# Performance work log

Measured on AMD Instinct MI355X. Metric: run time of the kernel, lower is better.

## Reference

```python
import jax, jax.numpy as jnp
import numpy as np

V = 100277      # VOCAB_SIZE
SCR = 64        # SCRATCH_SLOTS
STEPS = 8       # MAX_STEPS_LIMIT
H = 8           # num_heads (hard-coded in UniversalReasoner)
NEG = -1e9


def _layernorm(x, s, b, eps=1e-6):
    mu = x.mean(-1, keepdims=True)
    var = ((x - mu) ** 2).mean(-1, keepdims=True)
    return (x - mu) * jax.lax.rsqrt(var + eps) * s + b


def setup_inputs() -> dict:
    key = jax.random.key(0)
    ks = jax.random.split(key, 16)
    D = 1024
    n = lambda k, shape, sc=0.02: jax.random.normal(k, shape, dtype=jnp.float32) * sc
    return {
        "tokens": jax.random.randint(ks[0], (16, 128), 0, V),
        "embed": n(ks[1], (V, D)),
        "time_embed": n(ks[2], (STEPS + 1, D)),
        "scratch": n(ks[3], (1, SCR, D)),
        "wq": n(ks[4], (D, D)), "bq": jnp.zeros((D,), jnp.float32),
        "wk": n(ks[5], (D, D)), "bk": jnp.zeros((D,), jnp.float32),
        "wv": n(ks[6], (D, D)), "bv": jnp.zeros((D,), jnp.float32),
        "wo": n(ks[7], (D, D)), "bo": jnp.zeros((D,), jnp.float32),
        "ln1_s": jnp.ones((D,), jnp.float32), "ln1_b": jnp.zeros((D,), jnp.float32),
        "ln2_s": jnp.ones((D,), jnp.float32), "ln2_b": jnp.zeros((D,), jnp.float32),
        "w1": n(ks[8], (D, 4 * D)), "b1": jnp.zeros((4 * D,), jnp.float32),
        "w2": n(ks[9], (4 * D, D)), "b2": jnp.zeros((D,), jnp.float32),
        "halt_w": n(ks[10], (D, 1)), "halt_b": jnp.zeros((1,), jnp.float32),
        "dec_w": n(ks[11], (D, V)), "dec_b": jnp.zeros((V,), jnp.float32),
    }


def reference(tokens, embed, time_embed, scratch, wq, bq, wk, bk, wv, bv, wo, bo,
              ln1_s, ln1_b, ln2_s, ln2_b, w1, b1, w2, b2, halt_w, halt_b, dec_w, dec_b):
    B, S = tokens.shape
    D = embed.shape[1]
    hd = D // H
    T = S + SCR                     # seq + scratch slots
    scale = hd ** -0.5

    # RoPE caches (matches 10000**(arange(0,hd,2)/hd) in the module)
    inv_freq = 1.0 / 10000.0 ** (jnp.arange(0, hd, 2, dtype=jnp.float32) / hd)
    t = jnp.arange(T, dtype=jnp.float32)
    freqs = jnp.outer(t, inv_freq)              # [T, hd/2]
    sin = jnp.sin(freqs); cos = jnp.cos(freqs)
    sin_ext = jnp.stack([sin, sin], -1).reshape(T, hd)[None, :, None, :]
    cos_ext = jnp.stack([cos, cos], -1).reshape(T, hd)[None, :, None, :]

    # hybrid mask: causal for the seq part, fully-visible rows for scratch tokens
    causal = jnp.tril(jnp.ones((T, T), dtype=bool))
    mask = causal.at[S:, :].set(True)[None, None, :, :]   # [1,1,T,T]

    def rotate(x):  # x: [B,T,H,hd]
        xe, xo = x[..., 0::2], x[..., 1::2]
        xr = jnp.stack([-xo, xe], -1).reshape(x.shape)
        return x * cos_ext + xr * sin_ext

    def block(x):   # one StandardReasoningBlock on [B,T,D]
        h = _layernorm(x, ln1_s, ln1_b)
        q = (h @ wq + bq).reshape(B, T, H, hd)
        k = (h @ wk + bk).reshape(B, T, H, hd)
        v = (h @ wv + bv).reshape(B, T, H, hd)
        q, k = rotate(q), rotate(k)
        logits = jnp.einsum('bshd,bthd->bhst', q, k) * scale
        logits = jnp.where(mask, logits, NEG)
        w = jax.nn.softmax(logits, axis=-1)
        o = jnp.einsum('bhst,bthd->bshd', w, v).reshape(B, T, D)
        x = x + (o @ wo + bo)
        h2 = _layernorm(x, ln2_s, ln2_b)
        x = x + jax.nn.gelu(h2 @ w1 + b1, approximate=True) @ w2 + b2
        return x

    z0 = jnp.concatenate([embed[tokens], jnp.tile(scratch, (B, 1, 1))], axis=1)  # [B,T,D]

    def step(z, i):
        zt = z + time_embed[i][None, None, :]
        nz = block(zt)
        halt = jax.nn.sigmoid((nz[:, S:, :] @ halt_w + halt_b).mean(axis=(1, 2)))  # [B]
        return nz, halt

    final_z, halts = jax.lax.scan(step, z0, jnp.arange(STEPS))   # halts: [STEPS, B]
    logits_out = final_z[:, :S, :] @ dec_w + dec_b               # [B,S,V]
    return logits_out, halts
```

## Files before the change

kernel.cpp:

```cpp
#include <hip/hip_runtime.h>
#include <hip/hip_bf16.h>
#include <math.h>


typedef float  f32x4  __attribute__((ext_vector_type(4)));
typedef __bf16 bf16x8 __attribute__((ext_vector_type(8)));
typedef __bf16 bf16x4 __attribute__((ext_vector_type(4)));

static constexpr int BB   = 16;
static constexpr int S    = 128;
static constexpr int SCR  = 64;
static constexpr int T    = 192;
static constexpr int D    = 1024;
static constexpr int H    = 8;
static constexpr int HD   = 128;
static constexpr int DFF  = 4096;
static constexpr int NSTEP= 8;
static constexpr int V    = 100277;
static constexpr int ROWS = BB * T;
static constexpr int MD   = BB * S;
static constexpr long long LOGITS = (long long)BB * S * V;

#define DEV __device__ __forceinline__

DEV void gload16(const __bf16* g, __bf16* l) {
  __builtin_amdgcn_global_load_lds(
      (__attribute__((address_space(1))) void*)(g),
      (__attribute__((address_space(3))) void*)(l), 16, 0, 0);
}

template <int EPI>
__global__ __launch_bounds__(256) void k_gemm(
    const __bf16* __restrict__ A, long long sA, int ldA, int M,
    const __bf16* __restrict__ Bt, long long sB, int ldB, int N, int K,
    const float* __restrict__ bias, void* __restrict__ C, long long sC,
    int ldC) {
  const int bz = blockIdx.z;
  const __bf16* Ab;
  const __bf16* Bb;
  if constexpr (EPI == 4) {
    Ab = A + (size_t)bz * K;
    Bb = Bt + (size_t)bz * K;
  } else {
    Ab = A + (size_t)bz * sA;
    Bb = Bt + (size_t)bz * sB;
  }
  const int tm = blockIdx.y * 128, tn = blockIdx.x * 128;
  const int tid = threadIdx.x;
  const int lane = tid & 63, wv = tid >> 6;
  const int wr = wv >> 1, wc = wv & 1;

  __shared__ __bf16 As[2][128 * 32];
  __shared__ __bf16 Bs[2][128 * 32];

  f32x4 acc[4][4];
#pragma unroll
  for (int m = 0; m < 4; m++)
#pragma unroll
    for (int n = 0; n < 4; n++) acc[m][n] = (f32x4)(0.f);

  const int lrow = lane >> 2;
  const int lcol = (((lane & 3) ^ (lrow & 3)) * 8);
  int arow[2], brow[2];
#pragma unroll
  for (int c2 = 0; c2 < 2; c2++) {
    const int ch = wv * 2 + c2;
    int ar = tm + ch * 16 + lrow; if (ar > M - 1) ar = M - 1;
    int br = tn + ch * 16 + lrow; if (br > N - 1) br = N - 1;
    arow[c2] = ar; brow[c2] = br;
  }

  auto stage = [&](int buf, int kk) {
#pragma unroll
    for (int c2 = 0; c2 < 2; c2++) {
      const int ch = wv * 2 + c2;
      gload16(Ab + (size_t)arow[c2] * ldA + kk + lcol, &As[buf][ch * 512]);
      gload16(Bb + (size_t)brow[c2] * ldB + kk + lcol, &Bs[buf][ch * 512]);
    }
  };

  const int rsl = (((lane >> 4) ^ (lane & 3)) * 8);
  auto compute = [&](int cur) {
    bf16x8 af[4], bfv[4];
#pragma unroll
    for (int m = 0; m < 4; m++)
      af[m] = *(const bf16x8*)&As[cur][(wr * 64 + m * 16 + (lane & 15)) * 32 + rsl];
#pragma unroll
    for (int n = 0; n < 4; n++)
      bfv[n] = *(const bf16x8*)&Bs[cur][(wc * 64 + n * 16 + (lane & 15)) * 32 + rsl];
    asm volatile("s_waitcnt lgkmcnt(0)" ::: "memory");
    __builtin_amdgcn_sched_barrier(0);
    __builtin_amdgcn_s_barrier();
#pragma unroll
    for (int m = 0; m < 4; m++)
#pragma unroll
      for (int n = 0; n < 4; n++)
        acc[m][n] = __builtin_amdgcn_mfma_f32_16x16x32_bf16(af[m], bfv[n],
                                                            acc[m][n], 0, 0, 0);
  };

  const int niter = K >> 5;
  stage(0, 0);
  for (int it = 0; it < niter - 1; ++it) {
    const int cur = it & 1;
    stage(cur ^ 1, (it + 1) << 5);
    asm volatile("s_waitcnt vmcnt(4)" ::: "memory");
    __builtin_amdgcn_s_barrier();
    compute(cur);
  }
  asm volatile("s_waitcnt vmcnt(0)" ::: "memory");
  __builtin_amdgcn_s_barrier();
  compute((niter - 1) & 1);

  const int r0 = tm + wr * 64, c0 = tn + wc * 64;
#pragma unroll
  for (int n = 0; n < 4; n++) {
    const int c = c0 + n * 16 + (lane & 15);
    if (c >= N) continue;
    const float bsv = (bias && (EPI != 4 || bz == 0)) ? bias[c] : 0.f;
#pragma unroll
    for (int m = 0; m < 4; m++) {
      const int rb = r0 + m * 16 + ((lane >> 4) << 2);
#pragma unroll
      for (int j = 0; j < 4; j++) {
        const int r = rb + j;
        if (r >= M) continue;
        float x = acc[m][n][j] + bsv;
        if constexpr (EPI == 3) {
          const int b = bz >> 3, hh = bz & 7;
          ((__bf16*)C)[((size_t)(b * T + r)) * D + hh * HD + c] = (__bf16)x;
        } else if constexpr (EPI == 4) {
          atomicAdd((float*)C + (size_t)r * ldC + c, x);
        } else {
          const size_t idx = (size_t)bz * sC + (size_t)r * ldC + c;
          if constexpr (EPI == 2) {
            const float u = x;
            const float gl =
                0.5f * u * (1.f + tanhf(0.7978845608f * (u + 0.044715f * u * u * u)));
            ((__bf16*)C)[idx] = (__bf16)gl;
          } else if constexpr (EPI == 1) {
            ((float*)C)[idx] += x;
          } else {
            ((float*)C)[idx] = x;
          }
        }
      }
    }
  }
}

static constexpr int DEC_NT = (V + 127) / 128;
static constexpr int DEC_NWG = 16 * DEC_NT;

__global__ __launch_bounds__(256) void k_dec(const __bf16* __restrict__ A,
                                             const __bf16* __restrict__ Bt,
                                             const float* __restrict__ bias,
                                             float* __restrict__ C) {
  const int bid = blockIdx.x;
  const int swz = (bid & 7) * (DEC_NWG / 8) + (bid >> 3);
  const int tm = (swz & 15) * 128, tn = (swz >> 4) * 128;
  const int tid = threadIdx.x;
  const int lane = tid & 63, wv = tid >> 6;
  const int wr = wv >> 1, wc = wv & 1;

  __shared__ __bf16 sAB[2][2][4096];
  float* cbuf = (float*)sAB;

  f32x4 acc[4][4];
#pragma unroll
  for (int m = 0; m < 4; m++)
#pragma unroll
    for (int n = 0; n < 4; n++) acc[m][n] = (f32x4)(0.f);

  const int lrow = lane >> 2;
  const int lcol = (((lane & 3) ^ (lrow & 3)) * 8);
  int arow[2], brow[2];
#pragma unroll
  for (int c2 = 0; c2 < 2; c2++) {
    const int ch = wv * 2 + c2;
    arow[c2] = tm + ch * 16 + lrow;
    int br = tn + ch * 16 + lrow; if (br > V - 1) br = V - 1;
    brow[c2] = br;
  }

  auto stage = [&](int buf, int kk) {
#pragma unroll
    for (int c2 = 0; c2 < 2; c2++) {
      const int ch = wv * 2 + c2;
      gload16(A + (size_t)arow[c2] * D + kk + lcol, &sAB[buf][0][ch * 512]);
      gload16(Bt + (size_t)brow[c2] * D + kk + lcol, &sAB[buf][1][ch * 512]);
    }
  };

  const int rsl = (((lane >> 4) ^ (lane & 3)) * 8);
  auto compute = [&](int cur) {
    bf16x8 af[4], bfv[4];
#pragma unroll
    for (int m = 0; m < 4; m++)
      af[m] = *(const bf16x8*)&sAB[cur][0][(wr * 64 + m * 16 + (lane & 15)) * 32 + rsl];
#pragma unroll
    for (int n = 0; n < 4; n++)
      bfv[n] = *(const bf16x8*)&sAB[cur][1][(wc * 64 + n * 16 + (lane & 15)) * 32 + rsl];
    asm volatile("s_waitcnt lgkmcnt(0)" ::: "memory");
    __builtin_amdgcn_sched_barrier(0);
    __builtin_amdgcn_s_barrier();
#pragma unroll
    for (int m = 0; m < 4; m++)
#pragma unroll
      for (int n = 0; n < 4; n++)
        acc[m][n] = __builtin_amdgcn_mfma_f32_16x16x32_bf16(af[m], bfv[n],
                                                            acc[m][n], 0, 0, 0);
  };

  stage(0, 0);
  for (int it = 0; it < D / 32 - 1; ++it) {
    const int cur = it & 1;
    stage(cur ^ 1, (it + 1) << 5);
    asm volatile("s_waitcnt vmcnt(4)" ::: "memory");
    __builtin_amdgcn_s_barrier();
    compute(cur);
  }
  asm volatile("s_waitcnt vmcnt(0)" ::: "memory");
  __builtin_amdgcn_s_barrier();
  compute((D / 32 - 1) & 1);
  __syncthreads();

  const int l15 = lane & 15, g4 = lane >> 4;
  const bool full = (tn + 128 <= V);
  for (int pass = 0; pass < 2; ++pass) {
    if (pass) __syncthreads();
    if (wr == pass) {
#pragma unroll
      for (int n = 0; n < 4; n++) {
        const int col = wc * 64 + n * 16 + l15;
        const float bsv = (tn + col < V) ? bias[tn + col] : 0.f;
#pragma unroll
        for (int m = 0; m < 4; m++) {
#pragma unroll
          for (int j = 0; j < 4; j++) {
            const int row = m * 16 + g4 * 4 + j;
            const int slot = (col >> 2) ^ (row & 7);
            cbuf[row * 128 + slot * 4 + (col & 3)] = acc[m][n][j] + bsv;
          }
        }
      }
    }
    __syncthreads();
    const int rbase = tm + pass * 64;
    if (full) {
      const int c8 = tid & 7;
#pragma unroll
      for (int rr = 0; rr < 2; ++rr) {
        const int row = rr * 32 + (tid >> 3);
#pragma unroll
        for (int i = 0; i < 4; ++i) {
          const int ps = (c8 ^ (row & 7)) + i * 8;
          const f32x4 v = *(const f32x4*)&cbuf[row * 128 + ps * 4];
          *(f32x4*)&C[(size_t)(rbase + row) * V + tn + (c8 + i * 8) * 4] = v;
        }
      }
    } else {
      for (int idx = tid; idx < 64 * 128; idx += 256) {
        const int row = idx >> 7, col = idx & 127;
        if (tn + col < V)
          C[(size_t)(rbase + row) * V + tn + col] =
              cbuf[row * 128 + (((col >> 2) ^ (row & 7)) << 2) + (col & 3)];
      }
    }
  }
}

__global__ __launch_bounds__(256) void k_transpose(const float* __restrict__ in,
                                                   __bf16* __restrict__ out,
                                                   int R, int C) {
  __shared__ __bf16 tile[32][33];
  const int c0 = blockIdx.x * 32, r0 = blockIdx.y * 32;
  const int tx = threadIdx.x & 31, ty = threadIdx.x >> 5;
#pragma unroll
  for (int i = 0; i < 32; i += 8) {
    const int r = r0 + ty + i, c = c0 + tx;
    tile[ty + i][tx] = (r < R && c < C) ? (__bf16)in[(size_t)r * C + c] : (__bf16)0.f;
  }
  __syncthreads();
  const int oc = threadIdx.x >> 3, rch = (threadIdx.x & 7) * 4;
  const int occ = c0 + oc, orr = r0 + rch;
  if (occ < C && orr + 3 < R) {
    bf16x4 v;
#pragma unroll
    for (int j = 0; j < 4; j++) v[j] = tile[rch + j][oc];
    *(bf16x4*)(out + (size_t)occ * R + orr) = v;
  }
}

__global__ __launch_bounds__(256) void k_concat_bias(const float* bq,
                                                     const float* bk,
                                                     const float* bv,
                                                     float* out) {
  const int i = blockIdx.x * 256 + threadIdx.x;
  if (i < D) { out[i] = bq[i]; out[D + i] = bk[i]; out[2 * D + i] = bv[i]; }
}

__global__ __launch_bounds__(256) void k_rope_table(float* __restrict__ ct,
                                                    float* __restrict__ st) {
  const int i = blockIdx.x * 256 + threadIdx.x;
  if (i < T * 64) {
    const int t = i >> 6, j = i & 63;
    const float inv = expf(-((float)(2 * j) * (1.f / 128.f)) * 9.210340371976184f);
    const float ang = (float)t * inv;
    ct[i] = cosf(ang);
    st[i] = sinf(ang);
  }
}

__global__ __launch_bounds__(256) void k_build_z(const int* __restrict__ tokens,
                                                 const float* __restrict__ embed,
                                                 const float* __restrict__ scratch,
                                                 float* __restrict__ z) {
  const int row = blockIdx.x;
  const int b = row / T, t = row % T;
  const float* src = (t < S) ? embed + (size_t)tokens[b * S + t] * D
                             : scratch + (size_t)(t - S) * D;
  ((float4*)(z + (size_t)row * D))[threadIdx.x] =
      ((const float4*)src)[threadIdx.x];
}

template <bool ADDT>
__global__ __launch_bounds__(256) void k_ln(float* __restrict__ z,
                                            const float* __restrict__ te,
                                            const float* __restrict__ gs,
                                            const float* __restrict__ gb,
                                            __bf16* __restrict__ h) {
  const int row = blockIdx.x, tid = threadIdx.x;
  float* zp = z + (size_t)row * D;
  float4 x = ((float4*)zp)[tid];
  if (ADDT) {
    const float4 t4 = ((const float4*)te)[tid];
    x.x += t4.x; x.y += t4.y; x.z += t4.z; x.w += t4.w;
    ((float4*)zp)[tid] = x;
  }
  float s = x.x + x.y + x.z + x.w;
  float s2 = x.x * x.x + x.y * x.y + x.z * x.z + x.w * x.w;
#pragma unroll
  for (int o = 32; o; o >>= 1) { s += __shfl_xor(s, o); s2 += __shfl_xor(s2, o); }
  __shared__ float rs[4], rq[4];
  const int wv = tid >> 6, ln = tid & 63;
  if (!ln) { rs[wv] = s; rq[wv] = s2; }
  __syncthreads();
  s = rs[0] + rs[1] + rs[2] + rs[3];
  s2 = rq[0] + rq[1] + rq[2] + rq[3];
  const float mu = s * (1.f / D);
  const float var = s2 * (1.f / D) - mu * mu;
  const float rinv = 1.0f / sqrtf(var + 1e-6f);
  const int c = tid * 4;
  const float4 g4 = ((const float4*)gs)[tid];
  const float4 b4 = ((const float4*)gb)[tid];
  bf16x4 o4;
  o4[0] = (__bf16)((x.x - mu) * rinv * g4.x + b4.x);
  o4[1] = (__bf16)((x.y - mu) * rinv * g4.y + b4.y);
  o4[2] = (__bf16)((x.z - mu) * rinv * g4.z + b4.z);
  o4[3] = (__bf16)((x.w - mu) * rinv * g4.w + b4.w);
  *(bf16x4*)(h + (size_t)row * D + c) = o4;
}

__global__ __launch_bounds__(256) void k_rope_pack(
    const float* __restrict__ qkv, const float* __restrict__ ct,
    const float* __restrict__ st, __bf16* __restrict__ q,
    __bf16* __restrict__ k, __bf16* __restrict__ vT) {
  const int row = blockIdx.x;
  const int b = row / T, t = row % T;
  const int i0 = threadIdx.x * 4;
  const int hh = i0 >> 7, d = i0 & 127, j0 = d >> 1;
  const float* base = qkv + (size_t)row * 3072;
  const float4 qv = *(const float4*)(base + i0);
  const float4 kv = *(const float4*)(base + D + i0);
  const float4 vv = *(const float4*)(base + 2 * D + i0);
  const float c0 = ct[t * 64 + j0], s0 = st[t * 64 + j0];
  const float c1 = ct[t * 64 + j0 + 1], s1 = st[t * 64 + j0 + 1];
  bf16x4 qo, ko;
  qo[0] = (__bf16)(qv.x * c0 - qv.y * s0);
  qo[1] = (__bf16)(qv.y * c0 + qv.x * s0);
  qo[2] = (__bf16)(qv.z * c1 - qv.w * s1);
  qo[3] = (__bf16)(qv.w * c1 + qv.z * s1);
  ko[0] = (__bf16)(kv.x * c0 - kv.y * s0);
  ko[1] = (__bf16)(kv.y * c0 + kv.x * s0);
  ko[2] = (__bf16)(kv.z * c1 - kv.w * s1);
  ko[3] = (__bf16)(kv.w * c1 + kv.z * s1);
  const size_t ob = ((size_t)(b * H + hh) * T + t) * HD + d;
  *(bf16x4*)(q + ob) = qo;
  *(bf16x4*)(k + ob) = ko;
  const size_t vb = ((size_t)(b * H + hh) * HD + d) * T + t;
  vT[vb] = (__bf16)vv.x;
  vT[vb + T] = (__bf16)vv.y;
  vT[vb + 2 * T] = (__bf16)vv.z;
  vT[vb + 3 * T] = (__bf16)vv.w;
}

__global__ __launch_bounds__(256) void k_softmax(const float* __restrict__ sc,
                                                 __bf16* __restrict__ P) {
  const int wv = threadIdx.x >> 6, lane = threadIdx.x & 63;
  const int row = blockIdx.x * 4 + wv;
  const int tq = row % T;
  const int kmax = (tq < S) ? (tq + 1) : T;
  const float* srow = sc + (size_t)row * T;
  float v[3];
#pragma unroll
  for (int jj = 0; jj < 3; jj++) {
    const int idx = lane + 64 * jj;
    v[jj] = (idx < kmax) ? srow[idx] * 0.08838834764831845f : -1e30f;
  }
  float m = fmaxf(v[0], fmaxf(v[1], v[2]));
#pragma unroll
  for (int o = 32; o; o >>= 1) m = fmaxf(m, __shfl_xor(m, o));
  float e[3], ssum = 0.f;
#pragma unroll
  for (int jj = 0; jj < 3; jj++) { e[jj] = expf(v[jj] - m); ssum += e[jj]; }
#pragma unroll
  for (int o = 32; o; o >>= 1) ssum += __shfl_xor(ssum, o);
  const float inv = 1.f / ssum;
#pragma unroll
  for (int jj = 0; jj < 3; jj++)
    P[(size_t)row * T + lane + 64 * jj] = (__bf16)(e[jj] * inv);
}

__global__ __launch_bounds__(256) void k_halt(const float* __restrict__ z,
                                              const float* __restrict__ hw,
                                              const float* __restrict__ hb,
                                              float* __restrict__ out) {
  const int b = blockIdx.x, tid = threadIdx.x;
  const float4 w4 = ((const float4*)hw)[tid];
  float acc = 0.f;
  for (int j = 0; j < SCR; j++) {
    const float4 x = ((const float4*)(z + ((size_t)(b * T + S + j)) * D))[tid];
    acc += x.x * w4.x + x.y * w4.y + x.z * w4.z + x.w * w4.w;
  }
#pragma unroll
  for (int o = 32; o; o >>= 1) acc += __shfl_xor(acc, o);
  __shared__ float rs[4];
  const int wv = tid >> 6, ln = tid & 63;
  if (!ln) rs[wv] = acc;
  __syncthreads();
  if (tid == 0) {
    const float tot = rs[0] + rs[1] + rs[2] + rs[3];
    out[b] = 1.f / (1.f + expf(-(tot * (1.f / SCR) + hb[0])));
  }
}

__global__ __launch_bounds__(256) void k_cast(const float* __restrict__ z,
                                              __bf16* __restrict__ zb) {
  const int row = blockIdx.x;
  const int b = row >> 7, s = row & 127;
  const float4 x = ((const float4*)(z + ((size_t)(b * T + s)) * D))[threadIdx.x];
  bf16x4 o;
  o[0] = (__bf16)x.x; o[1] = (__bf16)x.y; o[2] = (__bf16)x.z; o[3] = (__bf16)x.w;
  *(bf16x4*)(zb + (size_t)row * D + threadIdx.x * 4) = o;
}

extern "C" void kernel_launch(void* const* d_in, const int* in_sizes, int n_in,
                              void* d_out, int out_size, void* d_ws,
                              size_t ws_size, hipStream_t stream) {
  const int* tokens = (const int*)d_in[0];
  const float* embed = (const float*)d_in[1];
  const float* time_embed = (const float*)d_in[2];
  const float* scratch = (const float*)d_in[3];
  const float* wq = (const float*)d_in[4];  const float* bq = (const float*)d_in[5];
  const float* wk = (const float*)d_in[6];  const float* bk = (const float*)d_in[7];
  const float* wvv = (const float*)d_in[8]; const float* bv = (const float*)d_in[9];
  const float* wo = (const float*)d_in[10]; const float* bo = (const float*)d_in[11];
  const float* ln1s = (const float*)d_in[12]; const float* ln1b = (const float*)d_in[13];
  const float* ln2s = (const float*)d_in[14]; const float* ln2b = (const float*)d_in[15];
  const float* w1 = (const float*)d_in[16]; const float* b1 = (const float*)d_in[17];
  const float* w2 = (const float*)d_in[18]; const float* b2 = (const float*)d_in[19];
  const float* hw = (const float*)d_in[20]; const float* hb = (const float*)d_in[21];
  const float* dw = (const float*)d_in[22]; const float* db = (const float*)d_in[23];

  char* w = (char*)d_ws;
  size_t off = 0;
  auto al = [&](size_t n) { size_t o = off; off += (n + 255) & ~(size_t)255; return o; };
  const size_t oWqkvT = al((size_t)3 * D * D * 2);
  const size_t oWoT   = al((size_t)D * D * 2);
  const size_t oW1T   = al((size_t)DFF * D * 2);
  const size_t oW2T   = al((size_t)D * DFF * 2);
  const size_t oDecT  = al((size_t)V * D * 2);
  const size_t oBqkv  = al((size_t)3 * D * 4);
  const size_t oCt    = al((size_t)T * 64 * 4);
  const size_t oSt    = al((size_t)T * 64 * 4);
  const size_t oZ     = al((size_t)ROWS * D * 4);
  const size_t oH     = al((size_t)ROWS * D * 2);
  const size_t oQKV   = al((size_t)ROWS * 3 * D * 4);
  const size_t oQ     = al((size_t)BB * H * T * HD * 2);
  const size_t oK     = al((size_t)BB * H * T * HD * 2);
  const size_t oVT    = al((size_t)BB * H * T * HD * 2);
  const size_t oSc    = al((size_t)BB * H * T * T * 4);
  const size_t oP     = al((size_t)BB * H * T * T * 2);
  (void)ws_size; (void)in_sizes; (void)n_in; (void)out_size;

  __bf16* WqkvT = (__bf16*)(w + oWqkvT);
  __bf16* WoT   = (__bf16*)(w + oWoT);
  __bf16* W1T   = (__bf16*)(w + oW1T);
  __bf16* W2T   = (__bf16*)(w + oW2T);
  __bf16* DecT  = (__bf16*)(w + oDecT);
  float*  bqkv  = (float*)(w + oBqkv);
  float*  ct    = (float*)(w + oCt);
  float*  st    = (float*)(w + oSt);
  float*  z     = (float*)(w + oZ);
  __bf16* h     = (__bf16*)(w + oH);
  float*  qkv   = (float*)(w + oQKV);
  __bf16* g     = (__bf16*)(w + oQKV);
  __bf16* ob    = (__bf16*)(w + oQKV + (size_t)ROWS * DFF * 2);
  __bf16* qb    = (__bf16*)(w + oQ);
  __bf16* kb    = (__bf16*)(w + oK);
  __bf16* vT    = (__bf16*)(w + oVT);
  float*  sc    = (float*)(w + oSc);
  __bf16* P     = (__bf16*)(w + oP);
  __bf16* zb    = (__bf16*)(w + oH);

  float* logits = (float*)d_out;
  float* halts  = (float*)d_out + LOGITS;

  k_transpose<<<dim3(32, 32), 256, 0, stream>>>(wq, WqkvT, D, D);
  k_transpose<<<dim3(32, 32), 256, 0, stream>>>(wk, WqkvT + (size_t)D * D, D, D);
  k_transpose<<<dim3(32, 32), 256, 0, stream>>>(wvv, WqkvT + (size_t)2 * D * D, D, D);
  k_transpose<<<dim3(32, 32), 256, 0, stream>>>(wo, WoT, D, D);
  k_transpose<<<dim3(128, 32), 256, 0, stream>>>(w1, W1T, D, DFF);
  k_transpose<<<dim3(32, 128), 256, 0, stream>>>(w2, W2T, DFF, D);
  k_transpose<<<dim3((V + 31) / 32, 32), 256, 0, stream>>>(dw, DecT, D, V);
  k_concat_bias<<<4, 256, 0, stream>>>(bq, bk, bv, bqkv);
  k_rope_table<<<(T * 64 + 255) / 256, 256, 0, stream>>>(ct, st);
  k_build_z<<<ROWS, 256, 0, stream>>>(tokens, embed, scratch, z);

  for (int step = 0; step < NSTEP; step++) {
    k_ln<true><<<ROWS, 256, 0, stream>>>(z, time_embed + (size_t)step * D, ln1s, ln1b, h);
    k_gemm<0><<<dim3(24, 24, 1), 256, 0, stream>>>(h, 0, D, ROWS, WqkvT, 0, D,
                                                   3 * D, D, bqkv, qkv, 0, 3 * D);
    k_rope_pack<<<ROWS, 256, 0, stream>>>(qkv, ct, st, qb, kb, vT);
    k_gemm<0><<<dim3(2, 2, BB * H), 256, 0, stream>>>(
        qb, (long long)T * HD, HD, T, kb, (long long)T * HD, HD, T, HD, nullptr,
        sc, (long long)T * T, T);
    k_softmax<<<BB * H * T / 4, 256, 0, stream>>>(sc, P);
    k_gemm<3><<<dim3(1, 2, BB * H), 256, 0, stream>>>(
        P, (long long)T * T, T, T, vT, (long long)HD * T, T, HD, T, nullptr,
        ob, 0, 0);
    k_gemm<1><<<dim3(8, 24, 1), 256, 0, stream>>>(ob, 0, D, ROWS, WoT, 0, D, D,
                                                  D, bo, z, 0, D);
    k_ln<false><<<ROWS, 256, 0, stream>>>(z, nullptr, ln2s, ln2b, h);
    k_gemm<2><<<dim3(32, 24, 1), 256, 0, stream>>>(h, 0, D, ROWS, W1T, 0, D,
                                                   DFF, D, b1, g, 0, DFF);
    k_gemm<4><<<dim3(8, 24, 4), 256, 0, stream>>>(g, 0, DFF, ROWS, W2T, 0, DFF,
                                                  D, DFF / 4, b2, z, 0, D);
    k_halt<<<BB, 256, 0, stream>>>(z, hw, hb, halts + step * BB);
  }

  k_cast<<<MD, 256, 0, stream>>>(z, zb);
  k_dec<<<DEC_NWG, 256, 0, stream>>>(zb, DecT, db, logits);
}
```

Measured before the change: 3.251 ms.

## Triple-buffer GEMM pipelines, change LDS swizzle, fuse RoPE packing into QKV epilogue

Both the generic GEMM and the decoder GEMM move from double to triple LDS buffering, prefetching two K-chunks ahead, and use a different XOR swizzle for LDS rows. The QKV projection gets a new epilogue that applies RoPE via lane shuffles and writes bf16 Q, K and transposed V directly. This removes the fp32 QKV intermediate and the separate rope_pack kernel. It costs more shared memory per block, which may reduce occupancy, and the epilogue's stores are more scattered.

```diff
diff --git a/kernel.cpp b/kernel.cpp
--- a/kernel.cpp
+++ b/kernel.cpp
@@ -20,6 +20,7 @@
 static constexpr int ROWS = BB * T;
 static constexpr int MD   = BB * S;
 static constexpr long long LOGITS = (long long)BB * S * V;
+static constexpr size_t QSZ = (size_t)BB * H * T * HD;
 
 #define DEV __device__ __forceinline__
 
@@ -34,7 +35,7 @@
     const __bf16* __restrict__ A, long long sA, int ldA, int M,
     const __bf16* __restrict__ Bt, long long sB, int ldB, int N, int K,
     const float* __restrict__ bias, void* __restrict__ C, long long sC,
-    int ldC) {
+    int ldC, const float* __restrict__ rct, const float* __restrict__ rst) {
   const int bz = blockIdx.z;
   const __bf16* Ab;
   const __bf16* Bb;
@@ -50,8 +51,8 @@
   const int lane = tid & 63, wv = tid >> 6;
   const int wr = wv >> 1, wc = wv & 1;
 
-  __shared__ __bf16 As[2][128 * 32];
-  __shared__ __bf16 Bs[2][128 * 32];
+  __shared__ __bf16 As[3][128 * 32];
+  __shared__ __bf16 Bs[3][128 * 32];
 
   f32x4 acc[4][4];
 #pragma unroll
@@ -60,7 +61,7 @@
     for (int n = 0; n < 4; n++) acc[m][n] = (f32x4)(0.f);
 
   const int lrow = lane >> 2;
-  const int lcol = (((lane & 3) ^ (lrow & 3)) * 8);
+  const int lcol = (((lane & 3) ^ ((lrow >> 1) & 3)) * 8);
   int arow[2], brow[2];
 #pragma unroll
   for (int c2 = 0; c2 < 2; c2++) {
@@ -79,7 +80,7 @@
     }
   };
 
-  const int rsl = (((lane >> 4) ^ (lane & 3)) * 8);
+  const int rsl = (((lane >> 4) ^ (((lane & 15) >> 1) & 3)) * 8);
   auto compute = [&](int cur) {
     bf16x8 af[4], bfv[4];
 #pragma unroll
@@ -101,18 +102,55 @@
 
   const int niter = K >> 5;
   stage(0, 0);
-  for (int it = 0; it < niter - 1; ++it) {
-    const int cur = it & 1;
-    stage(cur ^ 1, (it + 1) << 5);
-    asm volatile("s_waitcnt vmcnt(4)" ::: "memory");
+  stage(1, 32);
+  int cur = 0, nxt = 2;
+  for (int it = 0; it + 2 < niter; ++it) {
+    stage(nxt, (it + 2) << 5);
+    nxt = (nxt == 2) ? 0 : nxt + 1;
+    asm volatile("s_waitcnt vmcnt(8)" ::: "memory");
     __builtin_amdgcn_s_barrier();
     compute(cur);
-  }
+    cur = (cur == 2) ? 0 : cur + 1;
+  }
+  asm volatile("s_waitcnt vmcnt(4)" ::: "memory");
+  __builtin_amdgcn_s_barrier();
+  compute(cur);
+  cur = (cur == 2) ? 0 : cur + 1;
   asm volatile("s_waitcnt vmcnt(0)" ::: "memory");
   __builtin_amdgcn_s_barrier();
-  compute((niter - 1) & 1);
+  compute(cur);
 
   const int r0 = tm + wr * 64, c0 = tn + wc * 64;
+  if constexpr (EPI == 5) {
+    const int kind = tn >> 10;
+#pragma unroll
+    for (int n = 0; n < 4; n++) {
+      const int c = c0 + n * 16 + (lane & 15);
+      const int hh = (c & 1023) >> 7, d = c & 127, jp = d >> 1;
+      const float bsv = bias[c];
+#pragma unroll
+      for (int m = 0; m < 4; m++) {
+        const int rb = r0 + m * 16 + ((lane >> 4) << 2);
+#pragma unroll
+        for (int j = 0; j < 4; j++) {
+          const int r = rb + j;
+          const float x = acc[m][n][j] + bsv;
+          const float xo = __shfl_xor(x, 1);
+          const int b = r / T, t = r % T;
+          if (kind == 2) {
+            ((__bf16*)C)[2 * QSZ + ((size_t)((b * H + hh) * HD + d)) * T + t] =
+                (__bf16)x;
+          } else {
+            const float cs = rct[t * 64 + jp], sn = rst[t * 64 + jp];
+            const float o = (c & 1) ? (x * cs + xo * sn) : (x * cs - xo * sn);
+            ((__bf16*)C)[(size_t)kind * QSZ +
+                         ((size_t)((b * H + hh) * T + t)) * HD + d] = (__bf16)o;
+          }
+        }
+      }
+    }
+    return;
+  }
 #pragma unroll
   for (int n = 0; n < 4; n++) {
     const int c = c0 + n * 16 + (lane & 15);
@@ -163,7 +201,7 @@
   const int lane = tid & 63, wv = tid >> 6;
   const int wr = wv >> 1, wc = wv & 1;
 
-  __shared__ __bf16 sAB[2][2][4096];
+  __shared__ __bf16 sAB[3][2][4096];
   float* cbuf = (float*)sAB;
 
   f32x4 acc[4][4];
@@ -173,7 +211,7 @@
     for (int n = 0; n < 4; n++) acc[m][n] = (f32x4)(0.f);
 
   const int lrow = lane >> 2;
-  const int lcol = (((lane & 3) ^ (lrow & 3)) * 8);
+  const int lcol = (((lane & 3) ^ ((lrow >> 1) & 3)) * 8);
   int arow[2], brow[2];
 #pragma unroll
   for (int c2 = 0; c2 < 2; c2++) {
@@ -192,7 +230,7 @@
     }
   };
 
-  const int rsl = (((lane >> 4) ^ (lane & 3)) * 8);
+  const int rsl = (((lane >> 4) ^ (((lane & 15) >> 1) & 3)) * 8);
   auto compute = [&](int cur) {
     bf16x8 af[4], bfv[4];
 #pragma unroll
@@ -213,16 +251,23 @@
   };
 
   stage(0, 0);
-  for (int it = 0; it < D / 32 - 1; ++it) {
-    const int cur = it & 1;
-    stage(cur ^ 1, (it + 1) << 5);
-    asm volatile("s_waitcnt vmcnt(4)" ::: "memory");
+  stage(1, 32);
+  int cur = 0, nxt = 2;
+  for (int it = 0; it + 2 < D / 32; ++it) {
+    stage(nxt, (it + 2) << 5);
+    nxt = (nxt == 2) ? 0 : nxt + 1;
+    asm volatile("s_waitcnt vmcnt(8)" ::: "memory");
     __builtin_amdgcn_s_barrier();
     compute(cur);
-  }
+    cur = (cur == 2) ? 0 : cur + 1;
+  }
+  asm volatile("s_waitcnt vmcnt(4)" ::: "memory");
+  __builtin_amdgcn_s_barrier();
+  compute(cur);
+  cur = (cur == 2) ? 0 : cur + 1;
   asm volatile("s_waitcnt vmcnt(0)" ::: "memory");
   __builtin_amdgcn_s_barrier();
-  compute((D / 32 - 1) & 1);
+  compute(cur);
   __syncthreads();
 
   const int l15 = lane & 15, g4 = lane >> 4;
@@ -362,39 +407,6 @@
   *(bf16x4*)(h + (size_t)row * D + c) = o4;
 }
 
-__global__ __launch_bounds__(256) void k_rope_pack(
-    const float* __restrict__ qkv, const float* __restrict__ ct,
-    const float* __restrict__ st, __bf16* __restrict__ q,
-    __bf16* __restrict__ k, __bf16* __restrict__ vT) {
-  const int row = blockIdx.x;
-  const int b = row / T, t = row % T;
-  const int i0 = threadIdx.x * 4;
-  const int hh = i0 >> 7, d = i0 & 127, j0 = d >> 1;
-  const float* base = qkv + (size_t)row * 3072;
-  const float4 qv = *(const float4*)(base + i0);
-  const float4 kv = *(const float4*)(base + D + i0);
-  const float4 vv = *(const float4*)(base + 2 * D + i0);
-  const float c0 = ct[t * 64 + j0], s0 = st[t * 64 + j0];
-  const float c1 = ct[t * 64 + j0 + 1], s1 = st[t * 64 + j0 + 1];
-  bf16x4 qo, ko;
-  qo[0] = (__bf16)(qv.x * c0 - qv.y * s0);
-  qo[1] = (__bf16)(qv.y * c0 + qv.x * s0);
-  qo[2] = (__bf16)(qv.z * c1 - qv.w * s1);
-  qo[3] = (__bf16)(qv.w * c1 + qv.z * s1);
-  ko[0] = (__bf16)(kv.x * c0 - kv.y * s0);
-  ko[1] = (__bf16)(kv.y * c0 + kv.x * s0);
-  ko[2] = (__bf16)(kv.z * c1 - kv.w * s1);
-  ko[3] = (__bf16)(kv.w * c1 + kv.z * s1);
-  const size_t ob = ((size_t)(b * H + hh) * T + t) * HD + d;
-  *(bf16x4*)(q + ob) = qo;
-  *(bf16x4*)(k + ob) = ko;
-  const size_t vb = ((size_t)(b * H + hh) * HD + d) * T + t;
-  vT[vb] = (__bf16)vv.x;
-  vT[vb + T] = (__bf16)vv.y;
-  vT[vb + 2 * T] = (__bf16)vv.z;
-  vT[vb + 3 * T] = (__bf16)vv.w;
-}
-
 __global__ __launch_bounds__(256) void k_softmax(const float* __restrict__ sc,
                                                  __bf16* __restrict__ P) {
   const int wv = threadIdx.x >> 6, lane = threadIdx.x & 63;
@@ -486,10 +498,11 @@
   const size_t oSt    = al((size_t)T * 64 * 4);
   const size_t oZ     = al((size_t)ROWS * D * 4);
   const size_t oH     = al((size_t)ROWS * D * 2);
-  const size_t oQKV   = al((size_t)ROWS * 3 * D * 4);
-  const size_t oQ     = al((size_t)BB * H * T * HD * 2);
-  const size_t oK     = al((size_t)BB * H * T * HD * 2);
-  const size_t oVT    = al((size_t)BB * H * T * HD * 2);
+  const size_t oG     = al((size_t)ROWS * DFF * 2);
+  const size_t oOB    = al((size_t)ROWS * D * 2);
+  const size_t oQ     = al(QSZ * 2);
+  const size_t oK     = al(QSZ * 2);
+  const size_t oVT    = al(QSZ * 2);
   const size_t oSc    = al((size_t)BB * H * T * T * 4);
   const size_t oP     = al((size_t)BB * H * T * T * 2);
   (void)ws_size; (void)in_sizes; (void)n_in; (void)out_size;
@@ -504,9 +517,8 @@
   float*  st    = (float*)(w + oSt);
   float*  z     = (float*)(w + oZ);
   __bf16* h     = (__bf16*)(w + oH);
-  float*  qkv   = (float*)(w + oQKV);
-  __bf16* g     = (__bf16*)(w + oQKV);
-  __bf16* ob    = (__bf16*)(w + oQKV + (size_t)ROWS * DFF * 2);
+  __bf16* g     = (__bf16*)(w + oG);
+  __bf16* ob    = (__bf16*)(w + oOB);
   __bf16* qb    = (__bf16*)(w + oQ);
   __bf16* kb    = (__bf16*)(w + oK);
   __bf16* vT    = (__bf16*)(w + oVT);
@@ -530,23 +542,22 @@
 
   for (int step = 0; step < NSTEP; step++) {
     k_ln<true><<<ROWS, 256, 0, stream>>>(z, time_embed + (size_t)step * D, ln1s, ln1b, h);
-    k_gemm<0><<<dim3(24, 24, 1), 256, 0, stream>>>(h, 0, D, ROWS, WqkvT, 0, D,
-                                                   3 * D, D, bqkv, qkv, 0, 3 * D);
-    k_rope_pack<<<ROWS, 256, 0, stream>>>(qkv, ct, st, qb, kb, vT);
+    k_gemm<5><<<dim3(24, 24, 1), 256, 0, stream>>>(h, 0, D, ROWS, WqkvT, 0, D,
+                                                   3 * D, D, bqkv, qb, 0, 0, ct, st);
     k_gemm<0><<<dim3(2, 2, BB * H), 256, 0, stream>>>(
         qb, (long long)T * HD, HD, T, kb, (long long)T * HD, HD, T, HD, nullptr,
-        sc, (long long)T * T, T);
+        sc, (long long)T * T, T, nullptr, nullptr);
     k_softmax<<<BB * H * T / 4, 256, 0, stream>>>(sc, P);
     k_gemm<3><<<dim3(1, 2, BB * H), 256, 0, stream>>>(
         P, (long long)T * T, T, T, vT, (long long)HD * T, T, HD, T, nullptr,
-        ob, 0, 0);
+        ob, 0, 0, nullptr, nullptr);
     k_gemm<1><<<dim3(8, 24, 1), 256, 0, stream>>>(ob, 0, D, ROWS, WoT, 0, D, D,
-                                                  D, bo, z, 0, D);
+                                                  D, bo, z, 0, D, nullptr, nullptr);
     k_ln<false><<<ROWS, 256, 0, stream>>>(z, nullptr, ln2s, ln2b, h);
     k_gemm<2><<<dim3(32, 24, 1), 256, 0, stream>>>(h, 0, D, ROWS, W1T, 0, D,
-                                                   DFF, D, b1, g, 0, DFF);
+                                                   DFF, D, b1, g, 0, DFF, nullptr, nullptr);
     k_gemm<4><<<dim3(8, 24, 4), 256, 0, stream>>>(g, 0, DFF, ROWS, W2T, 0, DFF,
-                                                  D, DFF / 4, b2, z, 0, D);
+                                                  D, DFF / 4, b2, z, 0, D, nullptr, nullptr);
     k_halt<<<BB, 256, 0, stream>>>(z, hw, hb, halts + step * BB);
   }
 
```

Result: slower. 3.342 ms (+2.8%).
